# Optimization experiments

Hardware: AMD Instinct MI355X
Metric: run time of the kernel (lower is better)

Reference implementation:

```python
import jax, jax.numpy as jnp
import numpy as np

N_POINTS, N_TYPES, PER_TYPE, HIST, IN_U, U = 32768, 4, 8192, 32, 128, 128

def setup_inputs() -> dict:
    key = jax.random.key(0)
    ks = jax.random.split(key, 8)
    return {
        "current_node_state": jax.random.normal(ks[0], (N_POINTS, IN_U), jnp.float32),
        "historical_buffer": jax.random.normal(ks[1], (N_POINTS, HIST, U), jnp.float32),
        "entity_idx": jax.random.randint(ks[2], (N_TYPES, PER_TYPE), 0, N_POINTS, jnp.int32),
        "q_w": jax.random.normal(ks[3], (N_TYPES, IN_U, U), jnp.float32),
        "k_w": jax.random.normal(ks[4], (N_TYPES, U, U), jnp.float32),
        "v_w": jax.random.normal(ks[5], (N_TYPES, U, U), jnp.float32),
        "fc_w": jax.random.normal(ks[6], (N_TYPES, U, U), jnp.float32),
    }

def reference(current_node_state, historical_buffer, entity_idx, q_w, k_w, v_w, fc_w):
    # Batched-by-type gather (the original Python loop over entity types,
    # vectorized since all types have equal counts here).
    x = current_node_state[entity_idx]        # (T, N, IN_U)
    h = historical_buffer[entity_idx]         # (T, N, H, U)
    q = jnp.einsum('tne,teu->tnu', x, q_w)[:, :, None, :]   # (T, N, 1, U)
    k = jnp.einsum('tnhu,tuv->tnhv', h, k_w)                # (T, N, H, U)
    v = jnp.einsum('tnhu,tuv->tnhv', h, v_w)                # (T, N, H, U)
    raw = jnp.einsum('tnou,tnhu->tnoh', q, k)               # (T, N, 1, H)
    # NOTE: original uses F.softmax(raw_score) with implicit dim; for a 3D
    # tensor torch's legacy rule picks dim=0 (the per-type entity axis).
    attn = jax.nn.softmax(raw, axis=1)                      # softmax over N within each type
    agg = jnp.einsum('tnoh,tnhu->tnou', attn, v)            # (T, N, 1, U)
    out = jax.nn.relu(jnp.einsum('tnou,tuv->tnov', agg, fc_w)) + q
    # cat over types along node dim, then final squeeze -> (n_points, U)
    return out.reshape(N_TYPES * PER_TYPE, U)
```

## Files before the change

### kernel.cpp

```cpp
#include <hip/hip_runtime.h>
#include <math.h>

#define NPTS 32768
#define NTYPES 4
#define PER_TYPE 8192
#define HIST 32
#define UD 128
#define XT_STRIDE 36


__global__ __launch_bounds__(128) void prep_kernel(
    const float* __restrict__ k_w, const float* __restrict__ v_w,
    const float* __restrict__ fc_w, float* __restrict__ kT,
    float* __restrict__ wvf)
{
    int r = blockIdx.x;
    int t = blockIdx.y;
    int u = threadIdx.x;
    kT[(t * UD + r) * UD + u] = k_w[(t * UD + u) * UD + r];
    float acc = 0.f;
    const float* vrow = v_w + (t * UD + r) * UD;
    const float* fb = fc_w + t * UD * UD;
    #pragma unroll 8
    for (int m = 0; m < UD; ++m)
        acc = fmaf(vrow[m], fb[m * UD + u], acc);
    wvf[(t * UD + r) * UD + u] = acc;
}

__global__ __launch_bounds__(256) void qqk_kernel(
    const float* __restrict__ x, const int* __restrict__ idx,
    const float* __restrict__ q_w, const float* __restrict__ kT,
    float* __restrict__ q_out, float* __restrict__ qk_out)
{
    __shared__ float xT[UD * XT_STRIDE];
    __shared__ float qT[UD * XT_STRIDE];
    __shared__ int srow[32];
    int tx = threadIdx.x;
    int bn = blockIdx.x;
    int t  = blockIdx.y;
    int n0 = bn * 32;

    if (tx < 32) srow[tx] = idx[t * PER_TYPE + n0 + tx];
    __syncthreads();

    {
        int e = tx & 127;
        int half = tx >> 7;
        for (int i = 0; i < 16; ++i) {
            int ent = half * 16 + i;
            xT[e * XT_STRIDE + ent] = x[(size_t)srow[ent] * UD + e];
        }
    }
    __syncthreads();

    const int c4 = (tx & 31) * 4;
    const int eg = tx >> 5;
    float acc[4][4];

    #pragma unroll
    for (int i = 0; i < 4; ++i)
        #pragma unroll
        for (int j = 0; j < 4; ++j) acc[i][j] = 0.f;
    {
        const float* qw = q_w + t * UD * UD;
        for (int e = 0; e < UD; ++e) {
            float4 w = *(const float4*)(qw + e * UD + c4);
            float4 a0 = *(const float4*)(&xT[e * XT_STRIDE + eg * 4]);
            float av[4] = {a0.x, a0.y, a0.z, a0.w};
            #pragma unroll
            for (int i = 0; i < 4; ++i) {
                acc[i][0] = fmaf(av[i], w.x, acc[i][0]);
                acc[i][1] = fmaf(av[i], w.y, acc[i][1]);
                acc[i][2] = fmaf(av[i], w.z, acc[i][2]);
                acc[i][3] = fmaf(av[i], w.w, acc[i][3]);
            }
        }
    }
    #pragma unroll
    for (int i = 0; i < 4; ++i) {
        int g = t * PER_TYPE + n0 + eg * 4 + i;
        *(float4*)(q_out + (size_t)g * UD + c4) =
            make_float4(acc[i][0], acc[i][1], acc[i][2], acc[i][3]);
    }
    #pragma unroll
    for (int j = 0; j < 4; ++j) {
        *(float4*)(&qT[(c4 + j) * XT_STRIDE + eg * 4]) =
            make_float4(acc[0][j], acc[1][j], acc[2][j], acc[3][j]);
    }
    __syncthreads();

    #pragma unroll
    for (int i = 0; i < 4; ++i)
        #pragma unroll
        for (int j = 0; j < 4; ++j) acc[i][j] = 0.f;
    {
        const float* kw = kT + t * UD * UD;
        for (int v = 0; v < UD; ++v) {
            float4 w = *(const float4*)(kw + v * UD + c4);
            float4 a0 = *(const float4*)(&qT[v * XT_STRIDE + eg * 4]);
            float av[4] = {a0.x, a0.y, a0.z, a0.w};
            #pragma unroll
            for (int i = 0; i < 4; ++i) {
                acc[i][0] = fmaf(av[i], w.x, acc[i][0]);
                acc[i][1] = fmaf(av[i], w.y, acc[i][1]);
                acc[i][2] = fmaf(av[i], w.z, acc[i][2]);
                acc[i][3] = fmaf(av[i], w.w, acc[i][3]);
            }
        }
    }
    #pragma unroll
    for (int i = 0; i < 4; ++i) {
        int g = t * PER_TYPE + n0 + eg * 4 + i;
        *(float4*)(qk_out + (size_t)g * UD + c4) =
            make_float4(acc[i][0], acc[i][1], acc[i][2], acc[i][3]);
    }
}

__global__ __launch_bounds__(256) void raw_kernel(
    const float* __restrict__ hist, const int* __restrict__ idx,
    const float* __restrict__ qk, float* __restrict__ raw,
    float* __restrict__ pm, float* __restrict__ ps)
{
    __shared__ int srow[16];
    __shared__ float sqk[16 * UD];
    __shared__ float sm[HIST][2];
    __shared__ float ss[HIST][2];
    int tx = threadIdx.x;
    int bn = blockIdx.x;
    int t  = blockIdx.y;
    int n0 = bn * 16;
    if (tx < 16) srow[tx] = idx[t * PER_TYPE + n0 + tx];
    {
        int e = tx >> 4;
        int c = (tx & 15) * 8;
        const float* src = qk + ((size_t)(t * PER_TYPE + n0 + e)) * UD + c;
        float4 a = *(const float4*)(src);
        float4 b = *(const float4*)(src + 4);
        *(float4*)(&sqk[e * UD + c]) = a;
        *(float4*)(&sqk[e * UD + c + 4]) = b;
    }
    __syncthreads();

    int sub = tx & 3;
    int hh  = (tx >> 2) & 31;
    int eh  = tx >> 7;
    float m = -INFINITY, s = 0.f;
    for (int j = 0; j < 8; ++j) {
        int ei = j * 2 + eh;
        int g  = t * PER_TYPE + n0 + ei;
        const float* hr = hist + ((size_t)srow[ei] * HIST + hh) * UD + sub * 32;
        float4 h0 = *(const float4*)(hr);
        float4 h1 = *(const float4*)(hr + 4);
        float4 h2 = *(const float4*)(hr + 8);
        float4 h3 = *(const float4*)(hr + 12);
        float4 h4 = *(const float4*)(hr + 16);
        float4 h5 = *(const float4*)(hr + 20);
        float4 h6 = *(const float4*)(hr + 24);
        float4 h7 = *(const float4*)(hr + 28);
        const float* qr = &sqk[ei * UD + sub * 32];
        float4 q0 = *(const float4*)(qr);
        float4 q1 = *(const float4*)(qr + 4);
        float4 q2 = *(const float4*)(qr + 8);
        float4 q3 = *(const float4*)(qr + 12);
        float4 q4 = *(const float4*)(qr + 16);
        float4 q5 = *(const float4*)(qr + 20);
        float4 q6 = *(const float4*)(qr + 24);
        float4 q7 = *(const float4*)(qr + 28);
        float p0 = q0.x * h0.x + q0.y * h0.y + q0.z * h0.z + q0.w * h0.w;
        float p1 = q1.x * h1.x + q1.y * h1.y + q1.z * h1.z + q1.w * h1.w;
        float p2 = q2.x * h2.x + q2.y * h2.y + q2.z * h2.z + q2.w * h2.w;
        float p3 = q3.x * h3.x + q3.y * h3.y + q3.z * h3.z + q3.w * h3.w;
        p0 = fmaf(q4.x, h4.x, fmaf(q4.y, h4.y, fmaf(q4.z, h4.z, fmaf(q4.w, h4.w, p0))));
        p1 = fmaf(q5.x, h5.x, fmaf(q5.y, h5.y, fmaf(q5.z, h5.z, fmaf(q5.w, h5.w, p1))));
        p2 = fmaf(q6.x, h6.x, fmaf(q6.y, h6.y, fmaf(q6.z, h6.z, fmaf(q6.w, h6.w, p2))));
        p3 = fmaf(q7.x, h7.x, fmaf(q7.y, h7.y, fmaf(q7.z, h7.z, fmaf(q7.w, h7.w, p3))));
        float a = (p0 + p1) + (p2 + p3);
        a += __shfl_xor(a, 1);
        a += __shfl_xor(a, 2);
        if (sub == 0) raw[(size_t)g * HIST + hh] = a;
        float mo = m;
        m = fmaxf(m, a);
        s = s * __expf(mo - m) + __expf(a - m);
    }
    if (sub == 0) { sm[hh][eh] = m; ss[hh][eh] = s; }
    __syncthreads();
    if (tx < HIST) {
        float m0 = sm[tx][0], m1 = sm[tx][1];
        float M = fmaxf(m0, m1);
        float S = ss[tx][0] * __expf(m0 - M) + ss[tx][1] * __expf(m1 - M);
        pm[((size_t)t * HIST + tx) * 512 + bn] = M;
        ps[((size_t)t * HIST + tx) * 512 + bn] = S;
    }
}

__global__ __launch_bounds__(256) void merge_kernel(
    const float* __restrict__ pm, const float* __restrict__ ps,
    float* __restrict__ Mf, float* __restrict__ S)
{
    int b = blockIdx.x;
    int tx = threadIdx.x;
    float m = -INFINITY, s = 0.f;
    #pragma unroll
    for (int i = 0; i < 2; ++i) {
        int k = tx + i * 256;
        float pmv = pm[(size_t)b * 512 + k];
        float psv = ps[(size_t)b * 512 + k];
        float M = fmaxf(m, pmv);
        s = s * expf(m - M) + psv * expf(pmv - M);
        m = M;
    }
    #pragma unroll
    for (int off = 1; off < 64; off <<= 1) {
        float om = __shfl_xor(m, off);
        float os = __shfl_xor(s, off);
        float M = fmaxf(m, om);
        s = s * expf(m - M) + os * expf(om - M);
        m = M;
    }
    __shared__ float rm[4], rs[4];
    int wave = tx >> 6, lane = tx & 63;
    if (lane == 0) { rm[wave] = m; rs[wave] = s; }
    __syncthreads();
    if (tx == 0) {
        float M = fmaxf(fmaxf(rm[0], rm[1]), fmaxf(rm[2], rm[3]));
        float Sv = rs[0] * expf(rm[0] - M) + rs[1] * expf(rm[1] - M)
                 + rs[2] * expf(rm[2] - M) + rs[3] * expf(rm[3] - M);
        Mf[b] = M;
        S[b] = Sv;
    }
}

__global__ __launch_bounds__(256) void out_kernel(
    const float* __restrict__ hist, const int* __restrict__ idx,
    const float* __restrict__ q, const float* __restrict__ raw,
    const float* __restrict__ Mf, const float* __restrict__ S,
    const float* __restrict__ wvf, float* __restrict__ out)
{
    __shared__ float shbar[4][UD];
    int tx = threadIdx.x;
    int wave = tx >> 6;
    int lane = tx & 63;
    int g = blockIdx.x * 4 + wave;
    int t = g >> 13;
    float w = 0.f;
    if (lane < 32) {
        float r = raw[(size_t)g * HIST + lane];
        float M = Mf[t * HIST + lane];
        float e = r - M;
        if (e > -75.f) w = expf(e) / S[t * HIST + lane];
    }
    unsigned long long act = __ballot(w != 0.f);
    int u2 = lane * 2;
    float2 qv = *(const float2*)(q + (size_t)g * UD + u2);
    float2 o;
    if (act == 0ull) {
        o = qv;
    } else {
        int row = idx[g];
        float2 hb = make_float2(0.f, 0.f);
        unsigned long long m = act;
        while (m) {
            int hh = __ffsll(m) - 1;
            m &= m - 1;
            float wv = __shfl(w, hh);
            float2 hv = *(const float2*)(hist + ((size_t)row * HIST + hh) * UD + u2);
            hb.x = fmaf(wv, hv.x, hb.x);
            hb.y = fmaf(wv, hv.y, hb.y);
        }
        shbar[wave][u2] = hb.x;
        shbar[wave][u2 + 1] = hb.y;
        float2 a = make_float2(0.f, 0.f);
        const float* wt = wvf + t * UD * UD;
        for (int e = 0; e < UD; ++e) {
            float hbe = shbar[wave][e];
            float2 wr = *(const float2*)(wt + e * UD + u2);
            a.x = fmaf(hbe, wr.x, a.x);
            a.y = fmaf(hbe, wr.y, a.y);
        }
        o.x = fmaxf(a.x, 0.f) + qv.x;
        o.y = fmaxf(a.y, 0.f) + qv.y;
    }
    *(float2*)(out + (size_t)g * UD + u2) = o;
}

extern "C" void kernel_launch(void* const* d_in, const int* in_sizes, int n_in,
                              void* d_out, int out_size, void* d_ws, size_t ws_size,
                              hipStream_t stream) {
    const float* x    = (const float*)d_in[0];
    const float* hist = (const float*)d_in[1];
    const int*   idx  = (const int*)d_in[2];
    const float* q_w  = (const float*)d_in[3];
    const float* k_w  = (const float*)d_in[4];
    const float* v_w  = (const float*)d_in[5];
    const float* fc_w = (const float*)d_in[6];
    float* out = (float*)d_out;

    float* ws = (float*)d_ws;
    float* q     = ws;
    float* qk    = ws + 4194304;
    float* raw   = ws + 8388608;
    float* Mf    = ws + 9437184;
    float* S     = ws + 9437312;
    float* kT    = ws + 9437440;
    float* wvf   = ws + 9502976;
    float* pm    = ws + 9568512;
    float* ps    = ws + 9634048;

    prep_kernel<<<dim3(128, 4), 128, 0, stream>>>(k_w, v_w, fc_w, kT, wvf);
    qqk_kernel<<<dim3(256, 4), 256, 0, stream>>>(x, idx, q_w, kT, q, qk);
    raw_kernel<<<dim3(512, 4), 256, 0, stream>>>(hist, idx, qk, raw, pm, ps);
    merge_kernel<<<128, 256, 0, stream>>>(pm, ps, Mf, S);
    out_kernel<<<8192, 256, 0, stream>>>(hist, idx, q, raw, Mf, S, wvf, out);
}
```

Baseline: 747.9 us.

## Fuse q/qk projection into raw-score kernel, keeping qk in shared memory

Merges the q·Wq and q·Kᵀ projection kernel with the raw-score/partial-softmax kernel so the qk vectors stay in shared memory and never round-trip through global memory. The tile shrinks from 32 to 16 entities per block to match the raw kernel, with a new shared-memory stride and a 4-way unrolled inner loop. This removes one launch and the qk write/read, but halves reuse of the weight loads (q_w and kT are now re-read by twice as many blocks).

Result: no change. 756.4 us (+1.1%).

```diff
diff --git a/kernel.cpp b/kernel.cpp
--- a/kernel.cpp
+++ b/kernel.cpp
@@ -6,7 +6,7 @@
 #define PER_TYPE 8192
 #define HIST 32
 #define UD 128
-#define XT_STRIDE 36
+#define XSTR 17
 
 
 __global__ __launch_bounds__(128) void prep_kernel(
@@ -27,118 +27,129 @@
     wvf[(t * UD + r) * UD + u] = acc;
 }
 
-__global__ __launch_bounds__(256) void qqk_kernel(
+__global__ __launch_bounds__(256, 4) void qkr_kernel(
     const float* __restrict__ x, const int* __restrict__ idx,
     const float* __restrict__ q_w, const float* __restrict__ kT,
-    float* __restrict__ q_out, float* __restrict__ qk_out)
+    const float* __restrict__ hist,
+    float* __restrict__ q_out, float* __restrict__ raw,
+    float* __restrict__ pm, float* __restrict__ ps)
 {
-    __shared__ float xT[UD * XT_STRIDE];
-    __shared__ float qT[UD * XT_STRIDE];
-    __shared__ int srow[32];
+    __shared__ __align__(16) float xT[UD * XSTR];
+    __shared__ float qT[UD * XSTR];
+    __shared__ int srow[16];
+    __shared__ float sm[HIST][2], ss[HIST][2];
+
     int tx = threadIdx.x;
     int bn = blockIdx.x;
     int t  = blockIdx.y;
-    int n0 = bn * 32;
-
-    if (tx < 32) srow[tx] = idx[t * PER_TYPE + n0 + tx];
+    int n0 = bn * 16;
+
+    if (tx < 16) srow[tx] = idx[t * PER_TYPE + n0 + tx];
     __syncthreads();
 
     {
-        int e = tx & 127;
-        int half = tx >> 7;
-        for (int i = 0; i < 16; ++i) {
-            int ent = half * 16 + i;
-            xT[e * XT_STRIDE + ent] = x[(size_t)srow[ent] * UD + e];
-        }
+        int ent = tx & 15;
+        int cg  = tx >> 4;
+        const float* xr = x + (size_t)srow[ent] * UD + cg * 8;
+        float4 a = *(const float4*)(xr);
+        float4 b = *(const float4*)(xr + 4);
+        int c0 = cg * 8;
+        xT[(c0 + 0) * XSTR + ent] = a.x; xT[(c0 + 1) * XSTR + ent] = a.y;
+        xT[(c0 + 2) * XSTR + ent] = a.z; xT[(c0 + 3) * XSTR + ent] = a.w;
+        xT[(c0 + 4) * XSTR + ent] = b.x; xT[(c0 + 5) * XSTR + ent] = b.y;
+        xT[(c0 + 6) * XSTR + ent] = b.z; xT[(c0 + 7) * XSTR + ent] = b.w;
     }
     __syncthreads();
 
     const int c4 = (tx & 31) * 4;
-    const int eg = tx >> 5;
-    float acc[4][4];
-
-    #pragma unroll
-    for (int i = 0; i < 4; ++i)
+    const int e2 = (tx >> 5) * 2;
+    float acc[2][4];
+
+    #pragma unroll
+    for (int i = 0; i < 2; ++i)
         #pragma unroll
         for (int j = 0; j < 4; ++j) acc[i][j] = 0.f;
     {
         const float* qw = q_w + t * UD * UD;
-        for (int e = 0; e < UD; ++e) {
-            float4 w = *(const float4*)(qw + e * UD + c4);
-            float4 a0 = *(const float4*)(&xT[e * XT_STRIDE + eg * 4]);
-            float av[4] = {a0.x, a0.y, a0.z, a0.w};
-            #pragma unroll
-            for (int i = 0; i < 4; ++i) {
-                acc[i][0] = fmaf(av[i], w.x, acc[i][0]);
-                acc[i][1] = fmaf(av[i], w.y, acc[i][1]);
-                acc[i][2] = fmaf(av[i], w.z, acc[i][2]);
-                acc[i][3] = fmaf(av[i], w.w, acc[i][3]);
-            }
+        for (int e = 0; e < UD; e += 4) {
+            float4 w0 = *(const float4*)(qw + (e + 0) * UD + c4);
+            float4 w1 = *(const float4*)(qw + (e + 1) * UD + c4);
+            float4 w2 = *(const float4*)(qw + (e + 2) * UD + c4);
+            float4 w3 = *(const float4*)(qw + (e + 3) * UD + c4);
+            float x00 = xT[(e + 0) * XSTR + e2], x01 = xT[(e + 0) * XSTR + e2 + 1];
+            float x10 = xT[(e + 1) * XSTR + e2], x11 = xT[(e + 1) * XSTR + e2 + 1];
+            float x20 = xT[(e + 2) * XSTR + e2], x21 = xT[(e + 2) * XSTR + e2 + 1];
+            float x30 = xT[(e + 3) * XSTR + e2], x31 = xT[(e + 3) * XSTR + e2 + 1];
+            acc[0][0] = fmaf(x00, w0.x, acc[0][0]); acc[0][1] = fmaf(x00, w0.y, acc[0][1]);
+            acc[0][2] = fmaf(x00, w0.z, acc[0][2]); acc[0][3] = fmaf(x00, w0.w, acc[0][3]);
+            acc[1][0] = fmaf(x01, w0.x, acc[1][0]); acc[1][1] = fmaf(x01, w0.y, acc[1][1]);
+            acc[1][2] = fmaf(x01, w0.z, acc[1][2]); acc[1][3] = fmaf(x01, w0.w, acc[1][3]);
+            acc[0][0] = fmaf(x10, w1.x, acc[0][0]); acc[0][1] = fmaf(x10, w1.y, acc[0][1]);
+            acc[0][2] = fmaf(x10, w1.z, acc[0][2]); acc[0][3] = fmaf(x10, w1.w, acc[0][3]);
+            acc[1][0] = fmaf(x11, w1.x, acc[1][0]); acc[1][1] = fmaf(x11, w1.y, acc[1][1]);
+            acc[1][2] = fmaf(x11, w1.z, acc[1][2]); acc[1][3] = fmaf(x11, w1.w, acc[1][3]);
+            acc[0][0] = fmaf(x20, w2.x, acc[0][0]); acc[0][1] = fmaf(x20, w2.y, acc[0][1]);
+            acc[0][2] = fmaf(x20, w2.z, acc[0][2]); acc[0][3] = fmaf(x20, w2.w, acc[0][3]);
+            acc[1][0] = fmaf(x21, w2.x, acc[1][0]); acc[1][1] = fmaf(x21, w2.y, acc[1][1]);
+            acc[1][2] = fmaf(x21, w2.z, acc[1][2]); acc[1][3] = fmaf(x21, w2.w, acc[1][3]);
+            acc[0][0] = fmaf(x30, w3.x, acc[0][0]); acc[0][1] = fmaf(x30, w3.y, acc[0][1]);
+            acc[0][2] = fmaf(x30, w3.z, acc[0][2]); acc[0][3] = fmaf(x30, w3.w, acc[0][3]);
+            acc[1][0] = fmaf(x31, w3.x, acc[1][0]); acc[1][1] = fmaf(x31, w3.y, acc[1][1]);
+            acc[1][2] = fmaf(x31, w3.z, acc[1][2]); acc[1][3] = fmaf(x31, w3.w, acc[1][3]);
         }
     }
     #pragma unroll
-    for (int i = 0; i < 4; ++i) {
-        int g = t * PER_TYPE + n0 + eg * 4 + i;
+    for (int i = 0; i < 2; ++i) {
+        int g = t * PER_TYPE + n0 + e2 + i;
         *(float4*)(q_out + (size_t)g * UD + c4) =
             make_float4(acc[i][0], acc[i][1], acc[i][2], acc[i][3]);
     }
     #pragma unroll
     for (int j = 0; j < 4; ++j) {
-        *(float4*)(&qT[(c4 + j) * XT_STRIDE + eg * 4]) =
-            make_float4(acc[0][j], acc[1][j], acc[2][j], acc[3][j]);
-    }
-    __syncthreads();
-
-    #pragma unroll
-    for (int i = 0; i < 4; ++i)
+        qT[(c4 + j) * XSTR + e2]     = acc[0][j];
+        qT[(c4 + j) * XSTR + e2 + 1] = acc[1][j];
+    }
+    __syncthreads();
+
+    float* sqk = xT;
+    #pragma unroll
+    for (int i = 0; i < 2; ++i)
         #pragma unroll
         for (int j = 0; j < 4; ++j) acc[i][j] = 0.f;
     {
         const float* kw = kT + t * UD * UD;
-        for (int v = 0; v < UD; ++v) {
-            float4 w = *(const float4*)(kw + v * UD + c4);
-            float4 a0 = *(const float4*)(&qT[v * XT_STRIDE + eg * 4]);
-            float av[4] = {a0.x, a0.y, a0.z, a0.w};
-            #pragma unroll
-            for (int i = 0; i < 4; ++i) {
-                acc[i][0] = fmaf(av[i], w.x, acc[i][0]);
-                acc[i][1] = fmaf(av[i], w.y, acc[i][1]);
-                acc[i][2] = fmaf(av[i], w.z, acc[i][2]);
-                acc[i][3] = fmaf(av[i], w.w, acc[i][3]);
-            }
+        for (int v = 0; v < UD; v += 4) {
+            float4 w0 = *(const float4*)(kw + (v + 0) * UD + c4);
+            float4 w1 = *(const float4*)(kw + (v + 1) * UD + c4);
+            float4 w2 = *(const float4*)(kw + (v + 2) * UD + c4);
+            float4 w3 = *(const float4*)(kw + (v + 3) * UD + c4);
+            float x00 = qT[(v + 0) * XSTR + e2], x01 = qT[(v + 0) * XSTR + e2 + 1];
+            float x10 = qT[(v + 1) * XSTR + e2], x11 = qT[(v + 1) * XSTR + e2 + 1];
+            float x20 = qT[(v + 2) * XSTR + e2], x21 = qT[(v + 2) * XSTR + e2 + 1];
+            float x30 = qT[(v + 3) * XSTR + e2], x31 = qT[(v + 3) * XSTR + e2 + 1];
+            acc[0][0] = fmaf(x00, w0.x, acc[0][0]); acc[0][1] = fmaf(x00, w0.y, acc[0][1]);
+            acc[0][2] = fmaf(x00, w0.z, acc[0][2]); acc[0][3] = fmaf(x00, w0.w, acc[0][3]);
+            acc[1][0] = fmaf(x01, w0.x, acc[1][0]); acc[1][1] = fmaf(x01, w0.y, acc[1][1]);
+            acc[1][2] = fmaf(x01, w0.z, acc[1][2]); acc[1][3] = fmaf(x01, w0.w, acc[1][3]);
+            acc[0][0] = fmaf(x10, w1.x, acc[0][0]); acc[0][1] = fmaf(x10, w1.y, acc[0][1]);
+            acc[0][2] = fmaf(x10, w1.z, acc[0][2]); acc[0][3] = fmaf(x10, w1.w, acc[0][3]);
+            acc[1][0] = fmaf(x11, w1.x, acc[1][0]); acc[1][1] = fmaf(x11, w1.y, acc[1][1]);
+            acc[1][2] = fmaf(x11, w1.z, acc[1][2]); acc[1][3] = fmaf(x11, w1.w, acc[1][3]);
+            acc[0][0] = fmaf(x20, w2.x, acc[0][0]); acc[0][1] = fmaf(x20, w2.y, acc[0][1]);
+            acc[0][2] = fmaf(x20, w2.z, acc[0][2]); acc[0][3] = fmaf(x20, w2.w, acc[0][3]);
+            acc[1][0] = fmaf(x21, w2.x, acc[1][0]); acc[1][1] = fmaf(x21, w2.y, acc[1][1]);
+            acc[1][2] = fmaf(x21, w2.z, acc[1][2]); acc[1][3] = fmaf(x21, w2.w, acc[1][3]);
+            acc[0][0] = fmaf(x30, w3.x, acc[0][0]); acc[0][1] = fmaf(x30, w3.y, acc[0][1]);
+            acc[0][2] = fmaf(x30, w3.z, acc[0][2]); acc[0][3] = fmaf(x30, w3.w, acc[0][3]);
+            acc[1][0] = fmaf(x31, w3.x, acc[1][0]); acc[1][1] = fmaf(x31, w3.y, acc[1][1]);
+            acc[1][2] = fmaf(x31, w3.z, acc[1][2]); acc[1][3] = fmaf(x31, w3.w, acc[1][3]);
         }
     }
-    #pragma unroll
-    for (int i = 0; i < 4; ++i) {
-        int g = t * PER_TYPE + n0 + eg * 4 + i;
-        *(float4*)(qk_out + (size_t)g * UD + c4) =
+    __syncthreads();
+    #pragma unroll
+    for (int i = 0; i < 2; ++i)
+        *(float4*)(&sqk[(e2 + i) * UD + c4]) =
             make_float4(acc[i][0], acc[i][1], acc[i][2], acc[i][3]);
-    }
-}
-
-__global__ __launch_bounds__(256) void raw_kernel(
-    const float* __restrict__ hist, const int* __restrict__ idx,
-    const float* __restrict__ qk, float* __restrict__ raw,
-    float* __restrict__ pm, float* __restrict__ ps)
-{
-    __shared__ int srow[16];
-    __shared__ float sqk[16 * UD];
-    __shared__ float sm[HIST][2];
-    __shared__ float ss[HIST][2];
-    int tx = threadIdx.x;
-    int bn = blockIdx.x;
-    int t  = blockIdx.y;
-    int n0 = bn * 16;
-    if (tx < 16) srow[tx] = idx[t * PER_TYPE + n0 + tx];
-    {
-        int e = tx >> 4;
-        int c = (tx & 15) * 8;
-        const float* src = qk + ((size_t)(t * PER_TYPE + n0 + e)) * UD + c;
-        float4 a = *(const float4*)(src);
-        float4 b = *(const float4*)(src + 4);
-        *(float4*)(&sqk[e * UD + c]) = a;
-        *(float4*)(&sqk[e * UD + c + 4]) = b;
-    }
     __syncthreads();
 
     int sub = tx & 3;
@@ -187,9 +198,9 @@
     if (tx < HIST) {
         float m0 = sm[tx][0], m1 = sm[tx][1];
         float M = fmaxf(m0, m1);
-        float S = ss[tx][0] * __expf(m0 - M) + ss[tx][1] * __expf(m1 - M);
+        float Sv = ss[tx][0] * __expf(m0 - M) + ss[tx][1] * __expf(m1 - M);
         pm[((size_t)t * HIST + tx) * 512 + bn] = M;
-        ps[((size_t)t * HIST + tx) * 512 + bn] = S;
+        ps[((size_t)t * HIST + tx) * 512 + bn] = Sv;
     }
 }
 
@@ -297,7 +308,6 @@
 
     float* ws = (float*)d_ws;
     float* q     = ws;
-    float* qk    = ws + 4194304;
     float* raw   = ws + 8388608;
     float* Mf    = ws + 9437184;
     float* S     = ws + 9437312;
@@ -307,8 +317,7 @@
     float* ps    = ws + 9634048;
 
     prep_kernel<<<dim3(128, 4), 128, 0, stream>>>(k_w, v_w, fc_w, kT, wvf);
-    qqk_kernel<<<dim3(256, 4), 256, 0, stream>>>(x, idx, q_w, kT, q, qk);
-    raw_kernel<<<dim3(512, 4), 256, 0, stream>>>(hist, idx, qk, raw, pm, ps);
+    qkr_kernel<<<dim3(512, 4), 256, 0, stream>>>(x, idx, q_w, kT, hist, q, raw, pm, ps);
     merge_kernel<<<128, 256, 0, stream>>>(pm, ps, Mf, S);
     out_kernel<<<8192, 256, 0, stream>>>(hist, idx, q, raw, Mf, S, wvf, out);
 }
```
